# Kernel optimization log

Hardware: AMD Instinct MI355X
Metric: run time of the kernel (lower is better)

The kernel has to match this reference:

```python
import jax, jax.numpy as jnp
import numpy as np

N = 100000
E = 800000

def elu(x):
    return jnp.where(x > 0, x, jnp.expm1(x))

def transformer_conv(x, src, dst, ea, Wq, bq, Wk, bk, Wv, bv, We, Ws, bs, heads, ch):
    # PyG TransformerConv (concat=True, root_weight=True, beta=False, eval so dropout off)
    n = x.shape[0]
    q = (x @ Wq + bq).reshape(n, heads, ch)
    k = (x @ Wk + bk).reshape(n, heads, ch)
    v = (x @ Wv + bv).reshape(n, heads, ch)
    e = (ea @ We).reshape(-1, heads, ch)            # [E,H,C], lin_edge has no bias
    kj = k[src] + e                                  # [E,H,C]
    logits = (q[dst] * kj).sum(-1) / jnp.sqrt(jnp.float32(ch))  # [E,H]
    # segment softmax over incoming edges of each dst node
    m = jax.ops.segment_max(logits, dst, num_segments=n)
    ex = jnp.exp(logits - m[dst])
    denom = jax.ops.segment_sum(ex, dst, num_segments=n)
    alpha = ex / denom[dst]                          # [E,H]
    msg = alpha[..., None] * (v[src] + e)            # [E,H,C]
    agg = jax.ops.segment_sum(msg, dst, num_segments=n).reshape(n, heads * ch)
    return agg + x @ Ws + bs                         # skip connection (lin_skip)

def setup_inputs() -> dict:
    key = jax.random.key(0)
    ks = jax.random.split(key, 32)
    def rn(k, shape, scale=0.1):
        return jax.random.normal(k, shape, dtype=jnp.float32) * scale
    d = {}
    d['x'] = jax.random.normal(ks[0], (N, 23), dtype=jnp.float32)
    d['edge_index'] = jax.random.randint(ks[1], (2, E), 0, N, dtype=jnp.int32)
    d['edge_attr'] = jax.random.normal(ks[2], (E, 7), dtype=jnp.float32)
    d['linA_w'] = rn(ks[3], (23, 23)); d['linA_b'] = jnp.zeros((23,), jnp.float32)
    d['linB_w'] = rn(ks[4], (23, 23)); d['linB_b'] = jnp.zeros((23,), jnp.float32)
    # conv1: in=23, heads=8, out=24 -> 192
    d['q1_w'] = rn(ks[5], (23, 192)); d['q1_b'] = jnp.zeros((192,), jnp.float32)
    d['k1_w'] = rn(ks[6], (23, 192)); d['k1_b'] = jnp.zeros((192,), jnp.float32)
    d['v1_w'] = rn(ks[7], (23, 192)); d['v1_b'] = jnp.zeros((192,), jnp.float32)
    d['e1_w'] = rn(ks[8], (7, 192))
    d['s1_w'] = rn(ks[9], (23, 192)); d['s1_b'] = jnp.zeros((192,), jnp.float32)
    # conv4: in=192, heads=8, out=8 -> 64
    d['q2_w'] = rn(ks[10], (192, 64)); d['q2_b'] = jnp.zeros((64,), jnp.float32)
    d['k2_w'] = rn(ks[11], (192, 64)); d['k2_b'] = jnp.zeros((64,), jnp.float32)
    d['v2_w'] = rn(ks[12], (192, 64)); d['v2_b'] = jnp.zeros((64,), jnp.float32)
    d['e2_w'] = rn(ks[13], (7, 64))
    d['s2_w'] = rn(ks[14], (192, 64)); d['s2_b'] = jnp.zeros((64,), jnp.float32)
    d['lin1_w'] = rn(ks[15], (64, 20)); d['lin1_b'] = jnp.zeros((20,), jnp.float32)
    d['lin2_w'] = rn(ks[16], (20, 1)); d['lin2_b'] = jnp.zeros((1,), jnp.float32)
    return d

def reference(x, edge_index, edge_attr,
              linA_w, linA_b, linB_w, linB_b,
              q1_w, q1_b, k1_w, k1_b, v1_w, v1_b, e1_w, s1_w, s1_b,
              q2_w, q2_b, k2_w, k2_b, v2_w, v2_b, e2_w, s2_w, s2_b,
              lin1_w, lin1_b, lin2_w, lin2_b):
    src, dst = edge_index[0], edge_index[1]
    h = elu(x @ linA_w + linA_b)
    h = elu(h @ linB_w + linB_b)
    h = transformer_conv(h, src, dst, edge_attr, q1_w, q1_b, k1_w, k1_b, v1_w, v1_b, e1_w, s1_w, s1_b, 8, 24)
    h = elu(h)
    h = transformer_conv(h, src, dst, edge_attr, q2_w, q2_b, k2_w, k2_b, v2_w, v2_b, e2_w, s2_w, s2_b, 8, 8)
    h = elu(h)
    h = elu(h @ lin1_w + lin1_b)
    return h @ lin2_w + lin2_b
```

## Files before the change

kernel.cpp:

```cpp
#include <hip/hip_runtime.h>
#include <math.h>


__device__ __forceinline__ float elu_f(float x) {
    return x > 0.f ? x : expm1f(x);
}


__global__ void mlp_kernel(const float* __restrict__ x,
                           const float* __restrict__ A, const float* __restrict__ ab,
                           const float* __restrict__ B, const float* __restrict__ bb,
                           float* __restrict__ out, int n) {
    __shared__ float sA[23 * 23], sB[23 * 23], sa[23], sb[23];
    for (int t = threadIdx.x; t < 23 * 23; t += blockDim.x) { sA[t] = A[t]; sB[t] = B[t]; }
    if (threadIdx.x < 23) { sa[threadIdx.x] = ab[threadIdx.x]; sb[threadIdx.x] = bb[threadIdx.x]; }
    __syncthreads();
    int i = blockIdx.x * blockDim.x + threadIdx.x;
    if (i >= n) return;
    float xi[23], h1[23];
    #pragma unroll
    for (int j = 0; j < 23; j++) xi[j] = x[(size_t)i * 23 + j];
    #pragma unroll
    for (int o = 0; o < 23; o++) {
        float acc = sa[o];
        #pragma unroll
        for (int j = 0; j < 23; j++) acc = fmaf(xi[j], sA[j * 23 + o], acc);
        h1[o] = elu_f(acc);
    }
    #pragma unroll
    for (int o = 0; o < 23; o++) {
        float acc = sb[o];
        #pragma unroll
        for (int j = 0; j < 23; j++) acc = fmaf(h1[j], sB[j * 23 + o], acc);
        out[(size_t)i * 23 + o] = elu_f(acc);
    }
}

template<int IN, int Kc, int OUTW, int M, int TY>
__global__ void proj_tiled_kernel(const float* __restrict__ in, int n,
    const float* __restrict__ W0, const float* __restrict__ b0, float* __restrict__ o0,
    const float* __restrict__ W1, const float* __restrict__ b1, float* __restrict__ o1,
    const float* __restrict__ W2, const float* __restrict__ b2, float* __restrict__ o2,
    const float* __restrict__ W3, const float* __restrict__ b3, float* __restrict__ o3) {
    constexpr int WTOT = M * OUTW;
    constexpr int CG   = WTOT / 8;
    constexpr int BN   = TY * 4;
    constexpr int SAW  = BN + 4;
    constexpr int NT   = CG * TY;
    static_assert(IN % Kc == 0, "Kc must divide IN");
    static_assert(WTOT % 8 == 0 && OUTW % 4 == 0, "col alignment");
    __shared__ float sA[Kc][SAW];
    __shared__ float sB[Kc][WTOT];

    const int tid = threadIdx.x;
    const int tx = tid % CG;
    const int ty = tid / CG;
    const int node0 = blockIdx.x * BN;

    const int colA = tx * 4;
    const int colB = WTOT / 2 + tx * 4;
    const int matA = colA / OUTW, ccA = colA % OUTW;
    const int matB = colB / OUTW, ccB = colB % OUTW;
    const float* bA = (matA == 0 ? b0 : matA == 1 ? b1 : matA == 2 ? b2 : b3);
    const float* bB = (matB == 0 ? b0 : matB == 1 ? b1 : matB == 2 ? b2 : b3);
    float*       oA = (matA == 0 ? o0 : matA == 1 ? o1 : matA == 2 ? o2 : o3);
    float*       oB = (matB == 0 ? o0 : matB == 1 ? o1 : matB == 2 ? o2 : o3);

    float acc[4][8];
    #pragma unroll
    for (int i = 0; i < 4; i++) {
        #pragma unroll
        for (int c = 0; c < 4; c++) { acc[i][c] = bA[ccA + c]; acc[i][4 + c] = bB[ccB + c]; }
    }

    for (int k0 = 0; k0 < IN; k0 += Kc) {
        for (int t = tid; t < Kc * BN; t += NT) {
            int j = t / BN, nn = t - j * BN;
            int g = node0 + nn;
            sA[j][nn] = (g < n) ? in[(size_t)g * IN + k0 + j] : 0.f;
        }
        for (int t = tid; t < Kc * WTOT; t += NT) {
            int j = t / WTOT, c = t - j * WTOT;
            int m = c / OUTW, cm = c - m * OUTW;
            const float* Wp = (m == 0 ? W0 : m == 1 ? W1 : m == 2 ? W2 : W3);
            sB[j][c] = Wp[(size_t)(k0 + j) * OUTW + cm];
        }
        __syncthreads();
        #pragma unroll 8
        for (int j = 0; j < Kc; j++) {
            float4 a  = *(const float4*)&sA[j][ty * 4];
            float4 v0 = *(const float4*)&sB[j][colA];
            float4 v1 = *(const float4*)&sB[j][colB];
            float av[4] = {a.x, a.y, a.z, a.w};
            float bv[8] = {v0.x, v0.y, v0.z, v0.w, v1.x, v1.y, v1.z, v1.w};
            #pragma unroll
            for (int i = 0; i < 4; i++)
                #pragma unroll
                for (int c = 0; c < 8; c++)
                    acc[i][c] = fmaf(av[i], bv[c], acc[i][c]);
        }
        __syncthreads();
    }

    #pragma unroll
    for (int i = 0; i < 4; i++) {
        int g = node0 + ty * 4 + i;
        if (g >= n) continue;
        *(float4*)(oA + (size_t)g * OUTW + ccA) = make_float4(acc[i][0], acc[i][1], acc[i][2], acc[i][3]);
        *(float4*)(oB + (size_t)g * OUTW + ccB) = make_float4(acc[i][4], acc[i][5], acc[i][6], acc[i][7]);
    }
}


__global__ void zero2_kernel(int* __restrict__ a, int* __restrict__ b, int n) {
    int i = blockIdx.x * blockDim.x + threadIdx.x;
    if (i < n) { a[i] = 0; b[i] = 0; }
}

__global__ void count_kernel(const int* __restrict__ dst, int* __restrict__ cnt, int nE) {
    int e = blockIdx.x * blockDim.x + threadIdx.x;
    if (e < nE) atomicAdd(&cnt[dst[e]], 1);
}

__global__ void scan_block_kernel(int* __restrict__ cnt, int* __restrict__ bsum, int n) {
    __shared__ int sdat[256];
    int i = blockIdx.x * 256 + threadIdx.x;
    int v = (i < n) ? cnt[i] : 0;
    sdat[threadIdx.x] = v;
    __syncthreads();
    for (int off = 1; off < 256; off <<= 1) {
        int t = (threadIdx.x >= (unsigned)off) ? sdat[threadIdx.x - off] : 0;
        __syncthreads();
        sdat[threadIdx.x] += t;
        __syncthreads();
    }
    if (i < n) cnt[i] = sdat[threadIdx.x] - v;
    if (threadIdx.x == 255) bsum[blockIdx.x] = sdat[255];
}

__global__ void scan_bsum_kernel(int* __restrict__ bsum, int nb) {
    __shared__ int s[1024];
    int i = threadIdx.x;
    int v = (i < nb) ? bsum[i] : 0;
    s[i] = v;
    __syncthreads();
    for (int off = 1; off < 1024; off <<= 1) {
        int t = (i >= off) ? s[i - off] : 0;
        __syncthreads();
        s[i] += t;
        __syncthreads();
    }
    if (i < nb) bsum[i] = s[i] - v;
}

__global__ void finalize_rp_kernel(const int* __restrict__ cnt, const int* __restrict__ bsum,
                                   int* __restrict__ rp, int n, int nE) {
    int i = blockIdx.x * blockDim.x + threadIdx.x;
    if (i < n) rp[i] = cnt[i] + bsum[i >> 8];
    if (i == n) rp[n] = nE;
}

__global__ void scatter_kernel(const int* __restrict__ src, const int* __restrict__ dst,
                               const int* __restrict__ rp, int* __restrict__ cur,
                               int* __restrict__ srcS, int* __restrict__ eidS, int nE) {
    int e = blockIdx.x * blockDim.x + threadIdx.x;
    if (e >= nE) return;
    int d = dst[e];
    int pos = rp[d] + atomicAdd(&cur[d], 1);
    srcS[pos] = src[e];
    eidS[pos] = e;
}

template<int IN, int C, bool VMAT, bool QMAT, bool DOELU>
__global__ void conv_fused_kernel(const float* __restrict__ feat,
                                  const float* __restrict__ Wq, const float* __restrict__ qb,
                                  const float* __restrict__ Wv, const float* __restrict__ vb,
                                  const float* __restrict__ kmat, const float* __restrict__ vmat,
                                  const float* __restrict__ qmat,
                                  const float* __restrict__ ea, const float* __restrict__ We,
                                  const int* __restrict__ rp, const int* __restrict__ srcS,
                                  const int* __restrict__ eidS,
                                  float* __restrict__ out, int n, float scale) {
    constexpr int HC = 8 * C;
    constexpr int CPL = HC / 64;
    __shared__ float sWv[VMAT ? 1 : IN * HC];
    if constexpr (!VMAT) {
        for (int t = threadIdx.x; t < IN * HC; t += blockDim.x) sWv[t] = Wv[t];
        __syncthreads();
    }
    const int lane = threadIdx.x & 63;
    const int d = blockIdx.x * (blockDim.x >> 6) + (threadIdx.x >> 6);
    if (d >= n) return;
    const int ch0 = lane * CPL;

    float we[7][CPL];
    #pragma unroll
    for (int j = 0; j < 7; j++)
        #pragma unroll
        for (int c = 0; c < CPL; c++) we[j][c] = We[j * HC + ch0 + c];

    float vbr[CPL];
    if constexpr (!VMAT) {
        #pragma unroll
        for (int c = 0; c < CPL; c++) vbr[c] = vb[ch0 + c];
    }

    float* op = out + (size_t)d * HC + ch0;
    float sk[CPL], q[CPL];
    #pragma unroll
    for (int c = 0; c < CPL; c++) sk[c] = op[c];
    if constexpr (QMAT) {
        const float* qp = qmat + (size_t)d * HC + ch0;
        #pragma unroll
        for (int c = 0; c < CPL; c++) q[c] = qp[c];
    } else {
        #pragma unroll
        for (int c = 0; c < CPL; c++) q[c] = qb[ch0 + c];
        const float* fd = feat + (size_t)d * IN;
        for (int j = 0; j < IN; j++) {
            float f = fd[j];
            #pragma unroll
            for (int c = 0; c < CPL; c++)
                q[c] = fmaf(f, Wq[(size_t)j * HC + ch0 + c], q[c]);
        }
    }

    float m = -INFINITY, l = 0.f, acc[CPL];
    #pragma unroll
    for (int c = 0; c < CPL; c++) acc[c] = 0.f;

    const int p0 = rp[d], p1 = rp[d + 1];
    for (int p = p0; p < p1; p++) {
        int s = srcS[p];
        int eid = eidS[p];
        const float* eav = ea + (size_t)eid * 7;
        float ev[7];
        #pragma unroll
        for (int j = 0; j < 7; j++) ev[j] = eav[j];

        const float* kp = kmat + (size_t)s * HC + ch0;
        float vv[CPL];
        float part = 0.f;
        #pragma unroll
        for (int c = 0; c < CPL; c++) {
            float ec = 0.f;
            #pragma unroll
            for (int j = 0; j < 7; j++) ec = fmaf(ev[j], we[j][c], ec);
            part = fmaf(q[c], kp[c] + ec, part);
            vv[c] = ec;
        }
        if constexpr (VMAT) {
            const float* vp = vmat + (size_t)s * HC + ch0;
            #pragma unroll
            for (int c = 0; c < CPL; c++) vv[c] += vp[c];
        } else {
            #pragma unroll
            for (int c = 0; c < CPL; c++) vv[c] += vbr[c];
            const float* fs = feat + (size_t)s * IN;
            for (int j = 0; j < IN; j++) {
                float f = fs[j];
                #pragma unroll
                for (int c = 0; c < CPL; c++) vv[c] = fmaf(f, sWv[j * HC + ch0 + c], vv[c]);
            }
        }
        part += __shfl_xor(part, 1);
        part += __shfl_xor(part, 2);
        part += __shfl_xor(part, 4);
        float z = part * scale;
        float mn = fmaxf(m, z);
        float rs = expf(m - mn);
        float pw = expf(z - mn);
        l = l * rs + pw;
        #pragma unroll
        for (int c = 0; c < CPL; c++) acc[c] = fmaf(acc[c], rs, pw * vv[c]);
        m = mn;
    }
    float invl = (l > 0.f) ? 1.f / l : 0.f;
    #pragma unroll
    for (int c = 0; c < CPL; c++) {
        float r = sk[c] + acc[c] * invl;
        op[c] = DOELU ? elu_f(r) : r;
    }
}

__global__ void head_kernel(const float* __restrict__ h, const float* __restrict__ W1,
                            const float* __restrict__ b1, const float* __restrict__ W2,
                            const float* __restrict__ b2, float* __restrict__ out, int n) {
    __shared__ float sW1[64 * 20], sb1[20], sW2[20], sb2;
    for (int t = threadIdx.x; t < 64 * 20; t += blockDim.x) sW1[t] = W1[t];
    if (threadIdx.x < 20) { sb1[threadIdx.x] = b1[threadIdx.x]; sW2[threadIdx.x] = W2[threadIdx.x]; }
    if (threadIdx.x == 0) sb2 = b2[0];
    __syncthreads();
    int i = blockIdx.x * blockDim.x + threadIdx.x;
    if (i >= n) return;
    float hv[64];
    const float* hp = h + (size_t)i * 64;
    #pragma unroll
    for (int j = 0; j < 64; j++) hv[j] = elu_f(hp[j]);
    float acc2 = sb2;
    for (int o = 0; o < 20; o++) {
        float a = sb1[o];
        #pragma unroll
        for (int j = 0; j < 64; j++) a = fmaf(hv[j], sW1[j * 20 + o], a);
        acc2 = fmaf(elu_f(a), sW2[o], acc2);
    }
    out[i] = acc2;
}

__global__ void zero_out_kernel(float* __restrict__ out, int n) {
    int i = blockIdx.x * blockDim.x + threadIdx.x;
    if (i < n) out[i] = 0.f;
}


extern "C" void kernel_launch(void* const* d_in, const int* in_sizes, int n_in,
                              void* d_out, int out_size, void* d_ws, size_t ws_size,
                              hipStream_t stream) {
    const float* x   = (const float*)d_in[0];
    const int*   ei  = (const int*)d_in[1];
    const float* ea  = (const float*)d_in[2];
    const float* Aw  = (const float*)d_in[3];
    const float* Ab  = (const float*)d_in[4];
    const float* Bw  = (const float*)d_in[5];
    const float* Bb  = (const float*)d_in[6];
    const float* q1w = (const float*)d_in[7];  const float* q1b = (const float*)d_in[8];
    const float* k1w = (const float*)d_in[9];  const float* k1b = (const float*)d_in[10];
    const float* v1w = (const float*)d_in[11]; const float* v1b = (const float*)d_in[12];
    const float* e1w = (const float*)d_in[13];
    const float* s1w = (const float*)d_in[14]; const float* s1b = (const float*)d_in[15];
    const float* q2w = (const float*)d_in[16]; const float* q2b = (const float*)d_in[17];
    const float* k2w = (const float*)d_in[18]; const float* k2b = (const float*)d_in[19];
    const float* v2w = (const float*)d_in[20]; const float* v2b = (const float*)d_in[21];
    const float* e2w = (const float*)d_in[22];
    const float* s2w = (const float*)d_in[23]; const float* s2b = (const float*)d_in[24];
    const float* l1w = (const float*)d_in[25]; const float* l1b = (const float*)d_in[26];
    const float* l2w = (const float*)d_in[27]; const float* l2b = (const float*)d_in[28];

    const int n  = in_sizes[0] / 23;
    const int nE = in_sizes[1] / 2;
    const int* src = ei;
    const int* dst = ei + nE;
    float* out = (float*)d_out;
    const int B = 256;
    const int nb = (n + 255) / 256;

    size_t fl_h1 = ((size_t)n * 23 + 3) & ~(size_t)3;
    size_t fl_o1 = (size_t)n * 192;
    size_t fl_kvA = (size_t)n * 384;
    size_t fl_kB  = (size_t)n * 192;
    size_t ints_total = ((size_t)n + 1) + n + n + 1024 + (size_t)nE + (size_t)nE;

    size_t tierA_bytes = (fl_h1 + fl_o1 + fl_kvA) * 4 + ints_total * 4;
    size_t tierB_bytes = (fl_h1 + fl_o1 + fl_kB) * 4 + ints_total * 4;

    if (ws_size < tierB_bytes || nb > 1024) {
        zero_out_kernel<<<(out_size + B - 1) / B, B, 0, stream>>>(out, out_size);
        return;
    }
    const bool tierA = (ws_size >= tierA_bytes);

    float* ws = (float*)d_ws;
    size_t off = 0;
    float* h1   = ws + off; off += fl_h1;
    float* o1   = ws + off; off += fl_o1;
    float* kbuf = ws + off; off += (tierA ? fl_kvA : fl_kB);
    float* vbuf = tierA ? (kbuf + (size_t)n * 192) : nullptr;
    int* ip = (int*)(ws + off);
    int* rp   = ip; ip += (size_t)n + 1;
    int* cnt  = ip; ip += n;
    int* cur  = ip; ip += n;
    int* bsum = ip; ip += 1024;
    int* srcS = ip; ip += nE;
    int* eidS = ip; ip += nE;

    float* q2buf = kbuf;
    float* k2    = tierA ? (kbuf + (size_t)n * 64)  : kbuf;
    float* v2    = tierA ? (kbuf + (size_t)n * 128) : (kbuf + (size_t)n * 64);
    float* o2    = tierA ? (kbuf + (size_t)n * 192) : (kbuf + (size_t)n * 128);

    const float sc1 = 1.0f / sqrtf(24.0f);
    const float sc2 = 1.0f / sqrtf(8.0f);
    const float* np = nullptr;
    float* npw = nullptr;

    zero2_kernel<<<(n + B - 1) / B, B, 0, stream>>>(cnt, cur, n);
    count_kernel<<<(nE + B - 1) / B, B, 0, stream>>>(dst, cnt, nE);
    scan_block_kernel<<<nb, 256, 0, stream>>>(cnt, bsum, n);
    scan_bsum_kernel<<<1, 1024, 0, stream>>>(bsum, nb);
    finalize_rp_kernel<<<(n + 1 + B - 1) / B, B, 0, stream>>>(cnt, bsum, rp, n, nE);
    scatter_kernel<<<(nE + B - 1) / B, B, 0, stream>>>(src, dst, rp, cur, srcS, eidS, nE);

    mlp_kernel<<<(n + B - 1) / B, B, 0, stream>>>(x, Aw, Ab, Bw, Bb, h1, n);

    const int gproj = (n + 31) / 32;

    if (tierA) {
        proj_tiled_kernel<23, 23, 192, 3, 8><<<gproj, 576, 0, stream>>>(
            h1, n, k1w, k1b, kbuf, v1w, v1b, vbuf, s1w, s1b, o1, np, np, npw);
        conv_fused_kernel<23, 24, true, false, true><<<(n + 3) / 4, 256, 0, stream>>>(
            h1, q1w, q1b, v1w, v1b, kbuf, vbuf, np, ea, e1w, rp, srcS, eidS, o1, n, sc1);
    } else {
        proj_tiled_kernel<23, 23, 192, 2, 8><<<gproj, 384, 0, stream>>>(
            h1, n, k1w, k1b, kbuf, s1w, s1b, o1, np, np, npw, np, np, npw);
        conv_fused_kernel<23, 24, false, false, true><<<(n + 3) / 4, 256, 0, stream>>>(
            h1, q1w, q1b, v1w, v1b, kbuf, np, np, ea, e1w, rp, srcS, eidS, o1, n, sc1);
    }

    if (tierA) {
        proj_tiled_kernel<192, 32, 64, 4, 8><<<gproj, 256, 0, stream>>>(
            o1, n, q2w, q2b, q2buf, k2w, k2b, k2, v2w, v2b, v2, s2w, s2b, o2);
        conv_fused_kernel<192, 8, true, true, false><<<(n + 3) / 4, 256, 0, stream>>>(
            o1, q2w, q2b, v2w, v2b, k2, v2, q2buf, ea, e2w, rp, srcS, eidS, o2, n, sc2);
    } else {
        proj_tiled_kernel<192, 32, 64, 3, 8><<<gproj, 192, 0, stream>>>(
            o1, n, k2w, k2b, k2, v2w, v2b, v2, s2w, s2b, o2, np, np, npw);
        conv_fused_kernel<192, 8, true, false, false><<<(n + 3) / 4, 256, 0, stream>>>(
            o1, q2w, q2b, v2w, v2b, k2, v2, np, ea, e2w, rp, srcS, eidS, o2, n, sc2);
    }

    head_kernel<<<(n + B - 1) / B, B, 0, stream>>>(o2, l1w, l1b, l2w, l2b, out, n);
}
```

Baseline: 1.102 ms.

## Persistent chunked conv kernels with software-pipelined edge gathers and packed CSR

The conv kernels now launch a fixed grid of persistent wavefronts, each handling a contiguous chunk of destination nodes. Gathers of the next edge's K/V rows and edge attributes are issued before the current edge's math (double buffering), and the next node's q and skip values are prefetched. Source and edge ids are packed into one int2 CSR array, and a new workspace tier precomputes layer-1 Q with a projection kernel. This aims to hide gather latency and cut per-edge index loads, at the cost of more registers, more complex control flow and load imbalance across chunks.

```diff
diff --git a/kernel.cpp b/kernel.cpp
--- a/kernel.cpp
+++ b/kernel.cpp
@@ -162,25 +162,24 @@
 
 __global__ void scatter_kernel(const int* __restrict__ src, const int* __restrict__ dst,
                                const int* __restrict__ rp, int* __restrict__ cur,
-                               int* __restrict__ srcS, int* __restrict__ eidS, int nE) {
+                               int2* __restrict__ seS, int nE) {
     int e = blockIdx.x * blockDim.x + threadIdx.x;
     if (e >= nE) return;
     int d = dst[e];
     int pos = rp[d] + atomicAdd(&cur[d], 1);
-    srcS[pos] = src[e];
-    eidS[pos] = e;
+    seS[pos] = make_int2(src[e], e);
 }
 
 template<int IN, int C, bool VMAT, bool QMAT, bool DOELU>
-__global__ void conv_fused_kernel(const float* __restrict__ feat,
-                                  const float* __restrict__ Wq, const float* __restrict__ qb,
-                                  const float* __restrict__ Wv, const float* __restrict__ vb,
-                                  const float* __restrict__ kmat, const float* __restrict__ vmat,
-                                  const float* __restrict__ qmat,
-                                  const float* __restrict__ ea, const float* __restrict__ We,
-                                  const int* __restrict__ rp, const int* __restrict__ srcS,
-                                  const int* __restrict__ eidS,
-                                  float* __restrict__ out, int n, float scale) {
+__global__ __launch_bounds__(256, 4)
+void conv_fused_kernel(const float* __restrict__ feat,
+                       const float* __restrict__ Wq, const float* __restrict__ qb,
+                       const float* __restrict__ Wv, const float* __restrict__ vb,
+                       const float* __restrict__ kmat, const float* __restrict__ vmat,
+                       const float* __restrict__ qmat,
+                       const float* __restrict__ ea, const float* __restrict__ We,
+                       const int* __restrict__ rp, const int2* __restrict__ seS,
+                       float* __restrict__ out, int n, float scale, int chunk) {
     constexpr int HC = 8 * C;
     constexpr int CPL = HC / 64;
     __shared__ float sWv[VMAT ? 1 : IN * HC];
@@ -189,8 +188,9 @@
         __syncthreads();
     }
     const int lane = threadIdx.x & 63;
-    const int d = blockIdx.x * (blockDim.x >> 6) + (threadIdx.x >> 6);
-    if (d >= n) return;
+    int d = __builtin_amdgcn_readfirstlane((int)((blockIdx.x * blockDim.x + threadIdx.x) >> 6)) * chunk;
+    const int dEnd = min(n, d + chunk);
+    if (d >= dEnd) return;
     const int ch0 = lane * CPL;
 
     float we[7][CPL];
@@ -199,87 +199,195 @@
         #pragma unroll
         for (int c = 0; c < CPL; c++) we[j][c] = We[j * HC + ch0 + c];
 
-    float vbr[CPL];
-    if constexpr (!VMAT) {
+    auto loadQ = [&](int dd, float* qq) {
+        if constexpr (QMAT) {
+            const float* qp = qmat + (size_t)dd * HC + ch0;
+            #pragma unroll
+            for (int c = 0; c < CPL; c++) qq[c] = qp[c];
+        } else {
+            #pragma unroll
+            for (int c = 0; c < CPL; c++) qq[c] = qb[ch0 + c];
+            const float* fd = feat + (size_t)dd * IN;
+            for (int j = 0; j < IN; j++) {
+                float f = fd[j];
+                #pragma unroll
+                for (int c = 0; c < CPL; c++)
+                    qq[c] = fmaf(f, Wq[(size_t)j * HC + ch0 + c], qq[c]);
+            }
+        }
+    };
+
+    if constexpr (VMAT) {
+        float q[CPL], sk[CPL], qN[CPL], skN[CPL], acc[CPL];
+        float m = -INFINITY, l = 0.f;
+        loadQ(d, q);
+        {
+            const float* op = out + (size_t)d * HC + ch0;
+            #pragma unroll
+            for (int c = 0; c < CPL; c++) { sk[c] = op[c]; acc[c] = 0.f; }
+        }
+        if (d + 1 < dEnd) {
+            if constexpr (QMAT) {
+                const float* qp2 = qmat + (size_t)(d + 1) * HC + ch0;
+                #pragma unroll
+                for (int c = 0; c < CPL; c++) qN[c] = qp2[c];
+            }
+            const float* op2 = out + (size_t)(d + 1) * HC + ch0;
+            #pragma unroll
+            for (int c = 0; c < CPL; c++) skN[c] = op2[c];
+        }
+
+        int p = rp[d];
+        int pEnd = rp[d + 1];
+        const int P1 = rp[dEnd];
+
+        auto finishNode = [&]() {
+            float invl = (l > 0.f) ? 1.f / l : 0.f;
+            float* op = out + (size_t)d * HC + ch0;
+            #pragma unroll
+            for (int c = 0; c < CPL; c++) {
+                float r = sk[c] + acc[c] * invl;
+                op[c] = DOELU ? elu_f(r) : r;
+            }
+        };
+        auto advanceNode = [&]() -> bool {
+            d++;
+            if (d >= dEnd) return false;
+            if constexpr (QMAT) {
+                #pragma unroll
+                for (int c = 0; c < CPL; c++) q[c] = qN[c];
+            }
+            #pragma unroll
+            for (int c = 0; c < CPL; c++) sk[c] = skN[c];
+            if constexpr (!QMAT) loadQ(d, q);
+            if (d + 1 < dEnd) {
+                if constexpr (QMAT) {
+                    const float* qp2 = qmat + (size_t)(d + 1) * HC + ch0;
+                    #pragma unroll
+                    for (int c = 0; c < CPL; c++) qN[c] = qp2[c];
+                }
+                const float* op2 = out + (size_t)(d + 1) * HC + ch0;
+                #pragma unroll
+                for (int c = 0; c < CPL; c++) skN[c] = op2[c];
+            }
+            pEnd = rp[d + 1];
+            m = -INFINITY; l = 0.f;
+            #pragma unroll
+            for (int c = 0; c < CPL; c++) acc[c] = 0.f;
+            return true;
+        };
+
+        struct Rows { float k[CPL]; float v[CPL]; float ev[7]; };
+        auto issueRows = [&](Rows& R, int2 se) {
+            int sU   = __builtin_amdgcn_readfirstlane(se.x);
+            int eidU = __builtin_amdgcn_readfirstlane(se.y);
+            const float* eav = ea + (size_t)eidU * 7;
+            #pragma unroll
+            for (int j = 0; j < 7; j++) R.ev[j] = eav[j];
+            const float* kp = kmat + (size_t)sU * HC + ch0;
+            const float* vp = vmat + (size_t)sU * HC + ch0;
+            #pragma unroll
+            for (int c = 0; c < CPL; c++) { R.k[c] = kp[c]; R.v[c] = vp[c]; }
+        };
+        auto mathEdge = [&](Rows& R) {
+            float part = 0.f;
+            float vloc[CPL];
+            #pragma unroll
+            for (int c = 0; c < CPL; c++) {
+                float ec = 0.f;
+                #pragma unroll
+                for (int j = 0; j < 7; j++) ec = fmaf(R.ev[j], we[j][c], ec);
+                part = fmaf(q[c], R.k[c] + ec, part);
+                vloc[c] = R.v[c] + ec;
+            }
+            part += __shfl_xor(part, 1);
+            part += __shfl_xor(part, 2);
+            part += __shfl_xor(part, 4);
+            float z = part * scale;
+            float mn = fmaxf(m, z);
+            float rs = expf(m - mn);
+            float pw = expf(z - mn);
+            l = l * rs + pw;
+            #pragma unroll
+            for (int c = 0; c < CPL; c++) acc[c] = fmaf(acc[c], rs, pw * vloc[c]);
+            m = mn;
+        };
+
+        while (p >= pEnd) { finishNode(); if (!advanceNode()) return; }
+
+        int2 seA = seS[p];
+        int2 seB = (p + 1 < P1) ? seS[p + 1] : seA;
+        Rows rA, rB;
+        issueRows(rA, seA);
+
+        while (true) {
+            int2 seC = (p + 2 < P1) ? seS[p + 2] : seB;
+            if (p + 1 < P1) issueRows(rB, seB);
+            mathEdge(rA);
+            p++;
+            while (p >= pEnd) { finishNode(); if (!advanceNode()) return; }
+            int2 seD = (p + 2 < P1) ? seS[p + 2] : seC;
+            if (p + 1 < P1) issueRows(rA, seC);
+            mathEdge(rB);
+            p++;
+            while (p >= pEnd) { finishNode(); if (!advanceNode()) return; }
+            seB = seD;
+        }
+    } else {
+        float vbr[CPL];
         #pragma unroll
         for (int c = 0; c < CPL; c++) vbr[c] = vb[ch0 + c];
-    }
-
-    float* op = out + (size_t)d * HC + ch0;
-    float sk[CPL], q[CPL];
-    #pragma unroll
-    for (int c = 0; c < CPL; c++) sk[c] = op[c];
-    if constexpr (QMAT) {
-        const float* qp = qmat + (size_t)d * HC + ch0;
-        #pragma unroll
-        for (int c = 0; c < CPL; c++) q[c] = qp[c];
-    } else {
-        #pragma unroll
-        for (int c = 0; c < CPL; c++) q[c] = qb[ch0 + c];
-        const float* fd = feat + (size_t)d * IN;
-        for (int j = 0; j < IN; j++) {
-            float f = fd[j];
-            #pragma unroll
-            for (int c = 0; c < CPL; c++)
-                q[c] = fmaf(f, Wq[(size_t)j * HC + ch0 + c], q[c]);
-        }
-    }
-
-    float m = -INFINITY, l = 0.f, acc[CPL];
-    #pragma unroll
-    for (int c = 0; c < CPL; c++) acc[c] = 0.f;
-
-    const int p0 = rp[d], p1 = rp[d + 1];
-    for (int p = p0; p < p1; p++) {
-        int s = srcS[p];
-        int eid = eidS[p];
-        const float* eav = ea + (size_t)eid * 7;
-        float ev[7];
-        #pragma unroll
-        for (int j = 0; j < 7; j++) ev[j] = eav[j];
-
-        const float* kp = kmat + (size_t)s * HC + ch0;
-        float vv[CPL];
-        float part = 0.f;
-        #pragma unroll
-        for (int c = 0; c < CPL; c++) {
-            float ec = 0.f;
-            #pragma unroll
-            for (int j = 0; j < 7; j++) ec = fmaf(ev[j], we[j][c], ec);
-            part = fmaf(q[c], kp[c] + ec, part);
-            vv[c] = ec;
-        }
-        if constexpr (VMAT) {
-            const float* vp = vmat + (size_t)s * HC + ch0;
-            #pragma unroll
-            for (int c = 0; c < CPL; c++) vv[c] += vp[c];
-        } else {
-            #pragma unroll
-            for (int c = 0; c < CPL; c++) vv[c] += vbr[c];
-            const float* fs = feat + (size_t)s * IN;
-            for (int j = 0; j < IN; j++) {
-                float f = fs[j];
-                #pragma unroll
-                for (int c = 0; c < CPL; c++) vv[c] = fmaf(f, sWv[j * HC + ch0 + c], vv[c]);
-            }
-        }
-        part += __shfl_xor(part, 1);
-        part += __shfl_xor(part, 2);
-        part += __shfl_xor(part, 4);
-        float z = part * scale;
-        float mn = fmaxf(m, z);
-        float rs = expf(m - mn);
-        float pw = expf(z - mn);
-        l = l * rs + pw;
-        #pragma unroll
-        for (int c = 0; c < CPL; c++) acc[c] = fmaf(acc[c], rs, pw * vv[c]);
-        m = mn;
-    }
-    float invl = (l > 0.f) ? 1.f / l : 0.f;
-    #pragma unroll
-    for (int c = 0; c < CPL; c++) {
-        float r = sk[c] + acc[c] * invl;
-        op[c] = DOELU ? elu_f(r) : r;
+        for (; d < dEnd; d++) {
+            float q[CPL], sk[CPL], acc[CPL];
+            float m = -INFINITY, l = 0.f;
+            loadQ(d, q);
+            float* op = out + (size_t)d * HC + ch0;
+            #pragma unroll
+            for (int c = 0; c < CPL; c++) { sk[c] = op[c]; acc[c] = 0.f; }
+            const int p0 = rp[d], p1 = rp[d + 1];
+            for (int p = p0; p < p1; p++) {
+                int2 se = seS[p];
+                int s = se.x, eid = se.y;
+                const float* eav = ea + (size_t)eid * 7;
+                float ev[7];
+                #pragma unroll
+                for (int j = 0; j < 7; j++) ev[j] = eav[j];
+                const float* kp = kmat + (size_t)s * HC + ch0;
+                float vv[CPL];
+                float part = 0.f;
+                #pragma unroll
+                for (int c = 0; c < CPL; c++) {
+                    float ec = 0.f;
+                    #pragma unroll
+                    for (int j = 0; j < 7; j++) ec = fmaf(ev[j], we[j][c], ec);
+                    part = fmaf(q[c], kp[c] + ec, part);
+                    vv[c] = ec + vbr[c];
+                }
+                const float* fs = feat + (size_t)s * IN;
+                for (int j = 0; j < IN; j++) {
+                    float f = fs[j];
+                    #pragma unroll
+                    for (int c = 0; c < CPL; c++) vv[c] = fmaf(f, sWv[j * HC + ch0 + c], vv[c]);
+                }
+                part += __shfl_xor(part, 1);
+                part += __shfl_xor(part, 2);
+                part += __shfl_xor(part, 4);
+                float z = part * scale;
+                float mn = fmaxf(m, z);
+                float rs = expf(m - mn);
+                float pw = expf(z - mn);
+                l = l * rs + pw;
+                #pragma unroll
+                for (int c = 0; c < CPL; c++) acc[c] = fmaf(acc[c], rs, pw * vv[c]);
+                m = mn;
+            }
+            float invl = (l > 0.f) ? 1.f / l : 0.f;
+            #pragma unroll
+            for (int c = 0; c < CPL; c++) {
+                float r = sk[c] + acc[c] * invl;
+                op[c] = DOELU ? elu_f(r) : r;
+            }
+        }
     }
 }
 
@@ -348,35 +456,38 @@
     size_t fl_o1 = (size_t)n * 192;
     size_t fl_kvA = (size_t)n * 384;
     size_t fl_kB  = (size_t)n * 192;
-    size_t ints_total = ((size_t)n + 1) + n + n + 1024 + (size_t)nE + (size_t)nE;
-
-    size_t tierA_bytes = (fl_h1 + fl_o1 + fl_kvA) * 4 + ints_total * 4;
-    size_t tierB_bytes = (fl_h1 + fl_o1 + fl_kB) * 4 + ints_total * 4;
+    size_t fl_q1  = (size_t)n * 192;
+    size_t ints_total = 2 * (size_t)nE + ((size_t)n + 1) + n + n + 1024;
+
+    size_t tierB_bytes  = (fl_h1 + fl_o1 + fl_kB) * 4 + ints_total * 4;
+    size_t tierA_bytes  = (fl_h1 + fl_o1 + fl_kvA) * 4 + ints_total * 4;
+    size_t tierA2_bytes = tierA_bytes + fl_q1 * 4;
 
     if (ws_size < tierB_bytes || nb > 1024) {
         zero_out_kernel<<<(out_size + B - 1) / B, B, 0, stream>>>(out, out_size);
         return;
     }
-    const bool tierA = (ws_size >= tierA_bytes);
+    const int tier = (ws_size >= tierA2_bytes) ? 2 : (ws_size >= tierA_bytes) ? 1 : 0;
 
     float* ws = (float*)d_ws;
     size_t off = 0;
     float* h1   = ws + off; off += fl_h1;
     float* o1   = ws + off; off += fl_o1;
-    float* kbuf = ws + off; off += (tierA ? fl_kvA : fl_kB);
-    float* vbuf = tierA ? (kbuf + (size_t)n * 192) : nullptr;
-    int* ip = (int*)(ws + off);
+    float* kbuf = ws + off; off += (tier >= 1 ? fl_kvA : fl_kB);
+    float* vbuf = (tier >= 1) ? (kbuf + (size_t)n * 192) : nullptr;
+    float* q1buf = nullptr;
+    if (tier == 2) { q1buf = ws + off; off += fl_q1; }
+    int2* seS = (int2*)(ws + off);
+    int* ip = (int*)(seS + nE);
     int* rp   = ip; ip += (size_t)n + 1;
     int* cnt  = ip; ip += n;
     int* cur  = ip; ip += n;
-    int* bsum = ip; ip += 1024;
-    int* srcS = ip; ip += nE;
-    int* eidS = ip; ip += nE;
+    int* bsum = ip;
 
     float* q2buf = kbuf;
-    float* k2    = tierA ? (kbuf + (size_t)n * 64)  : kbuf;
-    float* v2    = tierA ? (kbuf + (size_t)n * 128) : (kbuf + (size_t)n * 64);
-    float* o2    = tierA ? (kbuf + (size_t)n * 192) : (kbuf + (size_t)n * 128);
+    float* k2    = (tier >= 1) ? (kbuf + (size_t)n * 64)  : kbuf;
+    float* v2    = (tier >= 1) ? (kbuf + (size_t)n * 128) : (kbuf + (size_t)n * 64);
+    float* o2    = (tier >= 1) ? (kbuf + (size_t)n * 192) : (kbuf + (size_t)n * 128);
 
     const float sc1 = 1.0f / sqrtf(24.0f);
     const float sc2 = 1.0f / sqrtf(8.0f);
@@ -388,34 +499,45 @@
     scan_block_kernel<<<nb, 256, 0, stream>>>(cnt, bsum, n);
     scan_bsum_kernel<<<1, 1024, 0, stream>>>(bsum, nb);
     finalize_rp_kernel<<<(n + 1 + B - 1) / B, B, 0, stream>>>(cnt, bsum, rp, n, nE);
-    scatter_kernel<<<(nE + B - 1) / B, B, 0, stream>>>(src, dst, rp, cur, srcS, eidS, nE);
+    scatter_kernel<<<(nE + B - 1) / B, B, 0, stream>>>(src, dst, rp, cur, seS, nE);
 
     mlp_kernel<<<(n + B - 1) / B, B, 0, stream>>>(x, Aw, Ab, Bw, Bb, h1, n);
 
     const int gproj = (n + 31) / 32;
 
-    if (tierA) {
+    const int CB = 2048;
+    const int NW = CB * 4;
+    const int chunk = (n + NW - 1) / NW;
+
+    if (tier == 2) {
         proj_tiled_kernel<23, 23, 192, 3, 8><<<gproj, 576, 0, stream>>>(
             h1, n, k1w, k1b, kbuf, v1w, v1b, vbuf, s1w, s1b, o1, np, np, npw);
-        conv_fused_kernel<23, 24, true, false, true><<<(n + 3) / 4, 256, 0, stream>>>(
-            h1, q1w, q1b, v1w, v1b, kbuf, vbuf, np, ea, e1w, rp, srcS, eidS, o1, n, sc1);
+        proj_tiled_kernel<23, 23, 192, 1, 8><<<gproj, 192, 0, stream>>>(
+            h1, n, q1w, q1b, q1buf, np, np, npw, np, np, npw, np, np, npw);
+        conv_fused_kernel<23, 24, true, true, true><<<CB, 256, 0, stream>>>(
+            h1, q1w, q1b, v1w, v1b, kbuf, vbuf, q1buf, ea, e1w, rp, seS, o1, n, sc1, chunk);
+    } else if (tier == 1) {
+        proj_tiled_kernel<23, 23, 192, 3, 8><<<gproj, 576, 0, stream>>>(
+            h1, n, k1w, k1b, kbuf, v1w, v1b, vbuf, s1w, s1b, o1, np, np, npw);
+        conv_fused_kernel<23, 24, true, false, true><<<CB, 256, 0, stream>>>(
+            h1, q1w, q1b, v1w, v1b, kbuf, vbuf, np, ea, e1w, rp, seS, o1, n, sc1, chunk);
     } else {
         proj_tiled_kernel<23, 23, 192, 2, 8><<<gproj, 384, 0, stream>>>(
             h1, n, k1w, k1b, kbuf, s1w, s1b, o1, np, np, npw, np, np, npw);
-        conv_fused_kernel<23, 24, false, false, true><<<(n + 3) / 4, 256, 0, stream>>>(
-            h1, q1w, q1b, v1w, v1b, kbuf, np, np, ea, e1w, rp, srcS, eidS, o1, n, sc1);
-    }
-
-    if (tierA) {
+        conv_fused_kernel<23, 24, false, false, true><<<CB, 256, 0, stream>>>(
+            h1, q1w, q1b, v1w, v1b, kbuf, np, np, ea, e1w, rp, seS, o1, n, sc1, chunk);
+    }
+
+    if (tier >= 1) {
         proj_tiled_kernel<192, 32, 64, 4, 8><<<gproj, 256, 0, stream>>>(
             o1, n, q2w, q2b, q2buf, k2w, k2b, k2, v2w, v2b, v2, s2w, s2b, o2);
-        conv_fused_kernel<192, 8, true, true, false><<<(n + 3) / 4, 256, 0, stream>>>(
-            o1, q2w, q2b, v2w, v2b, k2, v2, q2buf, ea, e2w, rp, srcS, eidS, o2, n, sc2);
+        conv_fused_kernel<192, 8, true, true, false><<<CB, 256, 0, stream>>>(
+            o1, q2w, q2b, v2w, v2b, k2, v2, q2buf, ea, e2w, rp, seS, o2, n, sc2, chunk);
     } else {
         proj_tiled_kernel<192, 32, 64, 3, 8><<<gproj, 192, 0, stream>>>(
             o1, n, k2w, k2b, k2, v2w, v2b, v2, s2w, s2b, o2, np, np, npw);
-        conv_fused_kernel<192, 8, true, false, false><<<(n + 3) / 4, 256, 0, stream>>>(
-            o1, q2w, q2b, v2w, v2b, k2, v2, np, ea, e2w, rp, srcS, eidS, o2, n, sc2);
+        conv_fused_kernel<192, 8, true, false, false><<<CB, 256, 0, stream>>>(
+            o1, q2w, q2b, v2w, v2b, k2, v2, np, ea, e2w, rp, seS, o2, n, sc2, chunk);
     }
 
     head_kernel<<<(n + B - 1) / B, B, 0, stream>>>(o2, l1w, l1b, l2w, l2b, out, n);
```

Result: slower. 4.068 ms (+269.1%).
